# Performance work log

Measured on AMD Instinct MI355X. Metric: run time of the kernel, lower is better.

The kernel has to match this reference:

```python
import jax, jax.numpy as jnp
import numpy as np

B, T, N, H = 1024, 256, 32, 64  # batch, SEQ_LEN, N_SERIES, RNN_HID_SIZE
EPS = 1e-05


def setup_inputs() -> dict:
    key = jax.random.key(0)
    ks = jax.random.split(key, 24)
    s_h = 1.0 / np.sqrt(H)
    s_n = 1.0 / np.sqrt(N)
    u = lambda k, shape, s: jax.random.uniform(k, shape, jnp.float32, -s, s)
    inp = {
        'values': jax.random.normal(ks[0], (B, T, N), jnp.float32),
        'masks': (jax.random.uniform(ks[1], (B, T, N)) < 0.8).astype(jnp.float32),
        'deltas': jax.random.uniform(ks[2], (B, T, N), jnp.float32) * 5.0,
        'evals': jax.random.normal(ks[3], (B, T, N), jnp.float32),
        'eval_masks': (jax.random.uniform(ks[4], (B, T, N)) < 0.1).astype(jnp.float32),
        'labels': (jax.random.uniform(ks[5], (B, 1)) < 0.5).astype(jnp.float32),
        'is_train': jnp.ones((B, 1), jnp.float32),
        # TemporalDecay h: Linear(N->H)
        'td_h_W': u(ks[6], (H, N), s_h), 'td_h_b': u(ks[7], (H,), s_h),
        # TemporalDecay x: diag Linear(N->N)
        'td_x_W': u(ks[8], (N, N), s_n), 'td_x_b': u(ks[9], (N,), s_n),
        # hist_reg: Linear(H->N)
        'hist_W': u(ks[10], (N, H), s_n), 'hist_b': u(ks[11], (N,), s_n),
        # feat_reg: masked Linear(N->N), mask = 1 - I
        'feat_W': u(ks[12], (N, N), s_n), 'feat_b': u(ks[13], (N,), s_n),
        # weight_combine: Linear(2N->N)
        'wc_W': u(ks[14], (N, 2 * N), s_n), 'wc_b': u(ks[15], (N,), s_n),
        # LSTMCell(2N -> H)
        'W_ih': u(ks[16], (4 * H, 2 * N), s_h), 'W_hh': u(ks[17], (4 * H, H), s_h),
        'b_ih': u(ks[18], (4 * H,), s_h), 'b_hh': u(ks[19], (4 * H,), s_h),
        # out: Linear(H->1)
        'out_W': u(ks[20], (1, H), s_h), 'out_b': u(ks[21], (1,), s_h),
    }
    return inp


def _rits_forward(values, masks, deltas, labels, is_train,
                  td_h_W, td_h_b, td_x_W, td_x_b, hist_W, hist_b,
                  feat_W, feat_b, wc_W, wc_b, W_ih, W_hh, b_ih, b_hh,
                  out_W, out_b):
    # time-major for scan: [T, B, N]
    vals_t = jnp.swapaxes(values, 0, 1)
    masks_t = jnp.swapaxes(masks, 0, 1)
    delts_t = jnp.swapaxes(deltas, 0, 1)

    feat_mask = 1.0 - jnp.eye(N, dtype=values.dtype)
    td_x_diag = jnp.diagonal(td_x_W)                  # W * eye(N) linear == elementwise diag

    def step(carry, xmd):
        h, c, x_loss = carry
        x, m, d = xmd
        gamma_h = jnp.exp(-jax.nn.relu(d @ td_h_W.T + td_h_b))   # [B,H]
        gamma_x = jnp.exp(-jax.nn.relu(d * td_x_diag + td_x_b))  # [B,N]
        h = h * gamma_h
        x_h = h @ hist_W.T + hist_b
        msum = jnp.sum(m) + EPS
        x_loss = x_loss + jnp.sum(jnp.abs(x - x_h) * m) / msum
        x_c = m * x + (1.0 - m) * x_h
        z_h = x_c @ (feat_W * feat_mask).T + feat_b
        x_loss = x_loss + jnp.sum(jnp.abs(x - z_h) * m) / msum
        alpha = jnp.concatenate([gamma_x, m], axis=1) @ wc_W.T + wc_b
        c_h = alpha * z_h + (1.0 - alpha) * x_h
        x_loss = x_loss + jnp.sum(jnp.abs(x - c_h) * m) / msum
        c_c = m * x + (1.0 - m) * c_h
        inputs = jnp.concatenate([c_c, m], axis=1)  # [B, 2N]
        gates = inputs @ W_ih.T + b_ih + h @ W_hh.T + b_hh
        i, f, g, o = jnp.split(gates, 4, axis=1)
        c = jax.nn.sigmoid(f) * c + jax.nn.sigmoid(i) * jnp.tanh(g)
        h = jax.nn.sigmoid(o) * jnp.tanh(c)
        return (h, c, x_loss), c_c

    h0 = jnp.zeros((values.shape[0], H), values.dtype)
    c0 = jnp.zeros((values.shape[0], H), values.dtype)
    (h, c, x_loss), imps = jax.lax.scan(step, (h0, c0, jnp.float32(0.0)),
                                        (vals_t, masks_t, delts_t))
    imputations = jnp.swapaxes(imps, 0, 1)  # [B, T, N]

    y_h = h @ out_W.T + out_b  # logits [B,1]
    # binary_cross_entropy_with_logits, reduce=False
    max_val = jnp.maximum(-y_h, 0.0)
    bce = y_h - y_h * labels + max_val + jnp.log(jnp.exp(-max_val) + jnp.exp(-y_h - max_val))
    y_loss = jnp.sum(bce * is_train) / (jnp.sum(is_train) + EPS)
    loss = x_loss / T + y_loss * 0.1
    predictions = jax.nn.sigmoid(y_h)
    return loss, predictions, imputations


def reference(values, masks, deltas, evals, eval_masks, labels, is_train,
              td_h_W, td_h_b, td_x_W, td_x_b, hist_W, hist_b, feat_W, feat_b,
              wc_W, wc_b, W_ih, W_hh, b_ih, b_hh, out_W, out_b):
    loss, predictions, imputations = _rits_forward(
        values, masks, deltas, labels, is_train,
        td_h_W, td_h_b, td_x_W, td_x_b, hist_W, hist_b,
        feat_W, feat_b, wc_W, wc_b, W_ih, W_hh, b_ih, b_hh, out_W, out_b)
    return loss, predictions, imputations
```

## Files before the change

### kernel.cpp

```cpp
#include <hip/hip_runtime.h>

#define EPSF 1e-5f

typedef _Float16 h2f  __attribute__((ext_vector_type(2)));
typedef _Float16 h8   __attribute__((ext_vector_type(8)));
typedef float    f32x4 __attribute__((ext_vector_type(4)));

#if defined(__has_builtin)
#if __has_builtin(__builtin_amdgcn_fdot2)
#define HAVE_FDOT2 1
#endif
#endif

__device__ __forceinline__ float fsig(float x){ return 1.0f/(1.0f+__expf(-x)); }
__device__ __forceinline__ float ftanh(float x){
  float e = __expf(2.f*x);
  float r = (e-1.f)/(e+1.f);
  return (x > 15.f) ? 1.f : ((x < -15.f) ? -1.f : r);
}
__device__ __forceinline__ int pkf(float lo, float hi){
  return __builtin_bit_cast(int, __builtin_amdgcn_cvt_pkrtz(lo, hi));
}
__device__ __forceinline__ int4 mk4(const float* p){
  return make_int4(pkf(p[0],p[1]),pkf(p[2],p[3]),pkf(p[4],p[5]),pkf(p[6],p[7]));
}
__device__ __forceinline__ float dot2(int w, int x, float acc){
#ifdef HAVE_FDOT2
  return __builtin_amdgcn_fdot2(__builtin_bit_cast(h2f, w),
                                __builtin_bit_cast(h2f, x), acc, false);
#else
  h2f a = __builtin_bit_cast(h2f, w), b = __builtin_bit_cast(h2f, x);
  return acc + (float)a[0]*(float)b[0] + (float)a[1]*(float)b[1];
#endif
}
__device__ __forceinline__ int rl_i(int v, int l){ return __builtin_amdgcn_readlane(v, l); }
__device__ __forceinline__ float rl_f(float v, int l){
  return __int_as_float(__builtin_amdgcn_readlane(__float_as_int(v), l));
}
#define BAR() do{ asm volatile("s_waitcnt lgkmcnt(0)" ::: "memory"); __builtin_amdgcn_s_barrier(); }while(0)

__global__ void msum_kernel(const float* __restrict__ masks, float* __restrict__ msum){
  const int t   = blockIdx.x;
  const int tid = threadIdx.x;
  const int b0  = tid >> 3;
  const int n4  = (tid & 7) << 2;
  float s = 0.f;
  #pragma unroll 4
  for (int i = 0; i < 32; ++i) {
    const int b = b0 + (i << 5);
    const float4 v = *reinterpret_cast<const float4*>(masks + ((size_t)b*256 + t)*32 + n4);
    s += v.x + v.y + v.z + v.w;
  }
  __shared__ float red[256];
  red[tid] = s; __syncthreads();
  for (int off = 128; off > 0; off >>= 1) {
    if (tid < off) red[tid] += red[tid + off];
    __syncthreads();
  }
  if (tid == 0) msum[t] = red[0] + EPSF;
}

__global__ __launch_bounds__(512)
__attribute__((amdgpu_waves_per_eu(2, 2)))
void rits_kernel(
  const float* __restrict__ values, const float* __restrict__ masks,
  const float* __restrict__ deltas, const float* __restrict__ labels,
  const float* __restrict__ is_train,
  const float* __restrict__ td_h_W, const float* __restrict__ td_h_b,
  const float* __restrict__ td_x_W, const float* __restrict__ td_x_b,
  const float* __restrict__ hist_W, const float* __restrict__ hist_b,
  const float* __restrict__ feat_W, const float* __restrict__ feat_b,
  const float* __restrict__ wc_W,  const float* __restrict__ wc_b,
  const float* __restrict__ W_ih,  const float* __restrict__ W_hh,
  const float* __restrict__ b_ih,  const float* __restrict__ b_hh,
  const float* __restrict__ out_W, const float* __restrict__ out_b,
  const float* __restrict__ msum,
  float* __restrict__ xl_acc, float* __restrict__ bce_acc,
  float* __restrict__ predictions, float* __restrict__ imps)
{
  __shared__ __align__(16) int  inp_s[4][84];
  __shared__ float gp[4][256];
  __shared__ float msum_l[256];

  const int tid = threadIdx.x;
  const int b   = blockIdx.x;
  const int wv  = tid >> 6;
  const int ln  = tid & 63;
  const bool chain = (wv < 4);
  const int me  = wv & 3;
  const int b2  = (b << 2) | me;

  if (tid < 256) msum_l[tid] = 1.0f / msum[tid];

  int4 Wb[2][4];
  const int kg = ln >> 4;
  #pragma unroll
  for (int nt = 0; nt < 2; ++nt){
    const int col = (wv << 5) + (nt << 4) + (ln & 15);
    #pragma unroll
    for (int ks = 0; ks < 4; ++ks){
      const int k0 = (ks << 5) + (kg << 3);
      const float* src = (k0 < 64) ? (W_ih + (size_t)col*64 + k0)
                                   : (W_hh + (size_t)col*64 + (k0 - 64));
      Wb[nt][ks] = make_int4(pkf(src[0],src[1]), pkf(src[2],src[3]),
                             pkf(src[4],src[5]), pkf(src[6],src[7]));
    }
  }
  const int col0 = (wv << 5) + (ln & 15);
  const float bs0 = b_ih[col0]      + b_hh[col0];
  const float bs1 = b_ih[col0 + 16] + b_hh[col0 + 16];

  int4  fB[4];
  int4  fC[8];
  int4  fDa[8];
  float wz[32];
  float thb_r=0.f, tdxd_r=0.f, tdxb_r=0.f, histb_r=0.f, featb_r=0.f, wcb_r=0.f;
  float xv=0.f, mv=0.f, dv=0.f;
  if (chain){
    const int nr = ln & 31;
    #pragma unroll
    for (int g = 0; g < 4; ++g) fB[g] = mk4(td_h_W + ln*32 + 8*g);
    #pragma unroll
    for (int g = 0; g < 8; ++g) fC[g] = mk4(hist_W + nr*64 + 8*g);
    #pragma unroll
    for (int g = 0; g < 8; ++g) fDa[g] = mk4(wc_W + nr*64 + 8*g);
    #pragma unroll
    for (int k = 0; k < 32; ++k) wz[k] = (k==nr) ? 0.f : feat_W[nr*32 + k];
    thb_r = td_h_b[ln];
    if (ln < 32){
      tdxd_r  = td_x_W[ln*33];
      tdxb_r  = td_x_b[ln];
      histb_r = hist_b[ln];
      featb_r = feat_b[ln];
      wcb_r   = wc_b[ln];
      const size_t base = (size_t)b2*8192 + ln;
      xv = values[base]; mv = masks[base]; dv = deltas[base];
    }
  }
  float h_reg = 0.f, c_reg = 0.f, loss_acc = 0.f;

  __syncthreads();

  for (int t = 0; t < 256; ++t){
    if (chain){
      const float x_cur = xv, m_cur = mv, d_cur = dv;
      float gx_r = 0.f;
      if (ln < 32){
        gx_r = __expf(-fmaxf(fmaf(d_cur, tdxd_r, tdxb_r), 0.f));
        if (t < 255){
          const size_t base = (size_t)b2*8192 + (size_t)(t+1)*32 + ln;
          xv = values[base]; mv = masks[base]; dv = deltas[base];
        }
      }
      const int i0 = (2*ln) & 63, i1 = (2*ln+1) & 63;
      const int dw = pkf(__shfl(d_cur, i0), __shfl(d_cur, i1));
      const int j0 = (2*ln-32) & 63, j1 = (2*ln-31) & 63;
      const float ga  = __shfl(gx_r,  i0), gb  = __shfl(gx_r,  i1);
      const float ma_ = __shfl(m_cur, j0), mb_ = __shfl(m_cur, j1);
      const int aw = (ln < 16) ? pkf(ga, gb) : pkf(ma_, mb_);

      {
        float a0 = thb_r, a1 = 0.f;
        #pragma unroll
        for (int g4 = 0; g4 < 4; ++g4){
          const int4 w = fB[g4];
          a0 = dot2(w.x, rl_i(dw, 4*g4+0), a0);
          a1 = dot2(w.y, rl_i(dw, 4*g4+1), a1);
          a0 = dot2(w.z, rl_i(dw, 4*g4+2), a0);
          a1 = dot2(w.w, rl_i(dw, 4*g4+3), a1);
        }
        h_reg *= __expf(-fmaxf(a0+a1, 0.f));
      }
      const int hw = pkf(__shfl(h_reg, i0), __shfl(h_reg, i1));
      float xh_v = 0.f, x_c_v = 0.f;
      if (ln < 32){
        float a0 = histb_r, a1 = 0.f, a2 = 0.f, a3 = 0.f;
        #pragma unroll
        for (int g4 = 0; g4 < 8; ++g4){
          const int4 w = fC[g4];
          a0 = dot2(w.x, rl_i(hw, 4*g4+0), a0);
          a1 = dot2(w.y, rl_i(hw, 4*g4+1), a1);
          a2 = dot2(w.z, rl_i(hw, 4*g4+2), a2);
          a3 = dot2(w.w, rl_i(hw, 4*g4+3), a3);
        }
        xh_v  = (a0+a1)+(a2+a3);
        x_c_v = m_cur*x_cur + (1.f-m_cur)*xh_v;
      }
      float ccv = 0.f;
      if (ln < 32){
        float z0 = featb_r, z1 = 0.f, z2 = 0.f, z3 = 0.f;
        #pragma unroll
        for (int k = 0; k < 32; k += 4){
          z0 = fmaf(rl_f(x_c_v, k+0), wz[k+0], z0);
          z1 = fmaf(rl_f(x_c_v, k+1), wz[k+1], z1);
          z2 = fmaf(rl_f(x_c_v, k+2), wz[k+2], z2);
          z3 = fmaf(rl_f(x_c_v, k+3), wz[k+3], z3);
        }
        const float z = (z0+z1)+(z2+z3);
        float a0 = wcb_r, a1 = 0.f, a2 = 0.f, a3 = 0.f;
        #pragma unroll
        for (int g4 = 0; g4 < 8; ++g4){
          const int4 w = fDa[g4];
          a0 = dot2(w.x, rl_i(aw, 4*g4+0), a0);
          a1 = dot2(w.y, rl_i(aw, 4*g4+1), a1);
          a2 = dot2(w.z, rl_i(aw, 4*g4+2), a2);
          a3 = dot2(w.w, rl_i(aw, 4*g4+3), a3);
        }
        const float al = (a0+a1)+(a2+a3);
        const float ch = al*z + (1.f-al)*xh_v;
        loss_acc += (fabsf(x_cur-xh_v)+fabsf(x_cur-z)+fabsf(x_cur-ch))*m_cur*msum_l[t];
        ccv = m_cur*x_cur + (1.f-m_cur)*ch;
        imps[(size_t)b2*8192 + (size_t)t*32 + ln] = ccv;
      }
      const int ccw = pkf(__shfl(ccv, i0), __shfl(ccv, i1));
      inp_s[me][ln] = (ln < 16) ? ccw : (ln < 32 ? aw : hw);
    }

    BAR();

    {
      const int arow = ln & 15;
      int4 A[4];
      if (arow < 4){
        #pragma unroll
        for (int ks = 0; ks < 4; ++ks)
          A[ks] = *reinterpret_cast<const int4*>(&inp_s[arow][(ks << 4) + (kg << 2)]);
      } else {
        #pragma unroll
        for (int ks = 0; ks < 4; ++ks) A[ks] = make_int4(0,0,0,0);
      }
      f32x4 acc0 = {bs0, bs0, bs0, bs0};
      f32x4 acc1 = {bs1, bs1, bs1, bs1};
      #pragma unroll
      for (int ks = 0; ks < 4; ++ks){
        acc0 = __builtin_amdgcn_mfma_f32_16x16x32_f16(
                 __builtin_bit_cast(h8, A[ks]), __builtin_bit_cast(h8, Wb[0][ks]), acc0, 0,0,0);
        acc1 = __builtin_amdgcn_mfma_f32_16x16x32_f16(
                 __builtin_bit_cast(h8, A[ks]), __builtin_bit_cast(h8, Wb[1][ks]), acc1, 0,0,0);
      }
      if (kg == 0){
        #pragma unroll
        for (int e = 0; e < 4; ++e){
          gp[e][col0]      = acc0[e];
          gp[e][col0 + 16] = acc1[e];
        }
      }
    }

    BAR();

    if (chain){
      const float ig = gp[me][ln];
      const float fg = gp[me][64+ln];
      const float gg = gp[me][128+ln];
      const float og = gp[me][192+ln];
      c_reg = fsig(fg)*c_reg + fsig(ig)*ftanh(gg);
      h_reg = fsig(og)*ftanh(c_reg);
    }
  }

  if (chain){
    float l = loss_acc;
    l += __shfl_xor(l,16); l += __shfl_xor(l,8);
    l += __shfl_xor(l,4);  l += __shfl_xor(l,2); l += __shfl_xor(l,1);
    if (ln == 0) atomicAdd(xl_acc, l);

    float p = h_reg * out_W[ln];
    p += __shfl_xor(p,32); p += __shfl_xor(p,16); p += __shfl_xor(p,8);
    p += __shfl_xor(p,4);  p += __shfl_xor(p,2);  p += __shfl_xor(p,1);
    if (ln == 0){
      const float y = p + out_b[0];
      predictions[b2] = fsig(y);
      const float lab = labels[b2];
      const float it  = is_train[b2];
      const float mx  = fmaxf(-y, 0.f);
      const float bce = y - y*lab + mx + __logf(__expf(-mx) + __expf(-y - mx));
      atomicAdd(bce_acc, bce * it);
    }
  }
}

__global__ void final_kernel(const float* __restrict__ is_train,
                             const float* __restrict__ ws,
                             float* __restrict__ out){
  const int tid = threadIdx.x;
  __shared__ float red[256];
  red[tid] = is_train[tid] + is_train[tid+256] + is_train[tid+512] + is_train[tid+768];
  __syncthreads();
  for (int off = 128; off > 0; off >>= 1){
    if (tid < off) red[tid] += red[tid + off];
    __syncthreads();
  }
  if (tid == 0){
    const float yl = ws[1] / (red[0] + EPSF);
    out[0] = ws[0] / 256.0f + 0.1f * yl;
  }
}

extern "C" void kernel_launch(void* const* d_in, const int* in_sizes, int n_in,
                              void* d_out, int out_size, void* d_ws, size_t ws_size,
                              hipStream_t stream){
  const float* values   = (const float*)d_in[0];
  const float* masks    = (const float*)d_in[1];
  const float* deltas   = (const float*)d_in[2];
  const float* labels   = (const float*)d_in[5];
  const float* is_train = (const float*)d_in[6];
  const float* td_h_W   = (const float*)d_in[7];
  const float* td_h_b   = (const float*)d_in[8];
  const float* td_x_W   = (const float*)d_in[9];
  const float* td_x_b   = (const float*)d_in[10];
  const float* hist_W   = (const float*)d_in[11];
  const float* hist_b   = (const float*)d_in[12];
  const float* feat_W   = (const float*)d_in[13];
  const float* feat_b   = (const float*)d_in[14];
  const float* wc_W     = (const float*)d_in[15];
  const float* wc_b     = (const float*)d_in[16];
  const float* W_ih     = (const float*)d_in[17];
  const float* W_hh     = (const float*)d_in[18];
  const float* b_ih     = (const float*)d_in[19];
  const float* b_hh     = (const float*)d_in[20];
  const float* out_W    = (const float*)d_in[21];
  const float* out_b    = (const float*)d_in[22];

  float* out = (float*)d_out;
  float* ws  = (float*)d_ws;

  hipMemsetAsync(ws, 0, 2*sizeof(float), stream);
  msum_kernel<<<256, 256, 0, stream>>>(masks, ws + 2);
  rits_kernel<<<256, 512, 0, stream>>>(values, masks, deltas, labels, is_train,
      td_h_W, td_h_b, td_x_W, td_x_b, hist_W, hist_b, feat_W, feat_b,
      wc_W, wc_b, W_ih, W_hh, b_ih, b_hh, out_W, out_b,
      ws + 2, ws + 0, ws + 1, out + 1, out + 1 + 1024);
  final_kernel<<<1, 256, 0, stream>>>(is_train, ws, out);
}
```

Measured before the change: 449.7 us.

## Offload temporal-decay hidden projection to idle waves via MFMA one step ahead

The td_h decay matmul (delta to H) moves off the serial chain waves. The non-chain waves (wv>=4) compute it with one MFMA per step for the next timestep, using packed deltas staged in shared memory. Chain waves now read the precomputed pre-activation from shared memory instead of doing 16 dot2+readlane ops on the critical path. This costs extra shared-memory traffic and an MFMA on the helper waves between the two barriers.

Measured after the change: 441.7 us. Within noise of the previous version (-1.8%).

```diff
diff --git a/kernel.cpp b/kernel.cpp
--- a/kernel.cpp
+++ b/kernel.cpp
@@ -37,6 +37,8 @@
 __device__ __forceinline__ float rl_f(float v, int l){
   return __int_as_float(__builtin_amdgcn_readlane(__float_as_int(v), l));
 }
+#define MFMA(A,B,C) __builtin_amdgcn_mfma_f32_16x16x32_f16( \
+    __builtin_bit_cast(h8,(A)), __builtin_bit_cast(h8,(B)), (C), 0,0,0)
 #define BAR() do{ asm volatile("s_waitcnt lgkmcnt(0)" ::: "memory"); __builtin_amdgcn_s_barrier(); }while(0)
 
 __global__ void msum_kernel(const float* __restrict__ masks, float* __restrict__ msum){
@@ -79,6 +81,8 @@
   float* __restrict__ predictions, float* __restrict__ imps)
 {
   __shared__ __align__(16) int  inp_s[4][84];
+  __shared__ __align__(16) int  dw_s[4][20];
+  __shared__ float sB[4][64];
   __shared__ float gp[4][256];
   __shared__ float msum_l[256];
 
@@ -89,11 +93,12 @@
   const bool chain = (wv < 4);
   const int me  = wv & 3;
   const int b2  = (b << 2) | me;
+  const int kg  = ln >> 4;
+  const int arow = ln & 15;
 
   if (tid < 256) msum_l[tid] = 1.0f / msum[tid];
 
   int4 Wb[2][4];
-  const int kg = ln >> 4;
   #pragma unroll
   for (int nt = 0; nt < 2; ++nt){
     const int col = (wv << 5) + (nt << 4) + (ln & 15);
@@ -110,23 +115,27 @@
   const float bs0 = b_ih[col0]      + b_hh[col0];
   const float bs1 = b_ih[col0 + 16] + b_hh[col0 + 16];
 
-  int4  fB[4];
+  int4 fGh = make_int4(0,0,0,0);
+  float ghb = 0.f; int colj = 0;
+  if (wv >= 4){
+    colj = ((wv - 4) << 4) | (ln & 15);
+    fGh  = mk4(td_h_W + colj*32 + kg*8);
+    ghb  = td_h_b[colj];
+  }
+
   int4  fC[8];
   int4  fDa[8];
   float wz[32];
-  float thb_r=0.f, tdxd_r=0.f, tdxb_r=0.f, histb_r=0.f, featb_r=0.f, wcb_r=0.f;
+  float tdxd_r=0.f, tdxb_r=0.f, histb_r=0.f, featb_r=0.f, wcb_r=0.f;
   float xv=0.f, mv=0.f, dv=0.f;
   if (chain){
     const int nr = ln & 31;
-    #pragma unroll
-    for (int g = 0; g < 4; ++g) fB[g] = mk4(td_h_W + ln*32 + 8*g);
     #pragma unroll
     for (int g = 0; g < 8; ++g) fC[g] = mk4(hist_W + nr*64 + 8*g);
     #pragma unroll
     for (int g = 0; g < 8; ++g) fDa[g] = mk4(wc_W + nr*64 + 8*g);
     #pragma unroll
     for (int k = 0; k < 32; ++k) wz[k] = (k==nr) ? 0.f : feat_W[nr*32 + k];
-    thb_r = td_h_b[ln];
     if (ln < 32){
       tdxd_r  = td_x_W[ln*33];
       tdxb_r  = td_x_b[ln];
@@ -138,12 +147,32 @@
     }
   }
   float h_reg = 0.f, c_reg = 0.f, loss_acc = 0.f;
-
+  const int i0 = (2*ln) & 63, i1 = (2*ln+1) & 63;
+  const int j0 = (2*ln-32) & 63, j1 = (2*ln-31) & 63;
+
+  __syncthreads();
+
+  if (chain){
+    const int dwn = pkf(__shfl(dv, i0), __shfl(dv, i1));
+    if (ln < 16) dw_s[me][ln] = dwn;
+  }
+  __syncthreads();
+  if (wv >= 4){
+    int4 A = make_int4(0,0,0,0);
+    if (arow < 4) A = *reinterpret_cast<const int4*>(&dw_s[arow][kg << 2]);
+    f32x4 acc = {ghb, ghb, ghb, ghb};
+    acc = MFMA(A, fGh, acc);
+    if (kg == 0){
+      #pragma unroll
+      for (int e = 0; e < 4; ++e) sB[e][colj] = acc[e];
+    }
+  }
   __syncthreads();
 
   for (int t = 0; t < 256; ++t){
     if (chain){
       const float x_cur = xv, m_cur = mv, d_cur = dv;
+      const float sb = sB[me][ln];
       float gx_r = 0.f;
       if (ln < 32){
         gx_r = __expf(-fmaxf(fmaf(d_cur, tdxd_r, tdxb_r), 0.f));
@@ -152,25 +181,11 @@
           xv = values[base]; mv = masks[base]; dv = deltas[base];
         }
       }
-      const int i0 = (2*ln) & 63, i1 = (2*ln+1) & 63;
-      const int dw = pkf(__shfl(d_cur, i0), __shfl(d_cur, i1));
-      const int j0 = (2*ln-32) & 63, j1 = (2*ln-31) & 63;
-      const float ga  = __shfl(gx_r,  i0), gb  = __shfl(gx_r,  i1);
+      const float ga  = __shfl(gx_r,  i0), gb_ = __shfl(gx_r,  i1);
       const float ma_ = __shfl(m_cur, j0), mb_ = __shfl(m_cur, j1);
-      const int aw = (ln < 16) ? pkf(ga, gb) : pkf(ma_, mb_);
-
-      {
-        float a0 = thb_r, a1 = 0.f;
-        #pragma unroll
-        for (int g4 = 0; g4 < 4; ++g4){
-          const int4 w = fB[g4];
-          a0 = dot2(w.x, rl_i(dw, 4*g4+0), a0);
-          a1 = dot2(w.y, rl_i(dw, 4*g4+1), a1);
-          a0 = dot2(w.z, rl_i(dw, 4*g4+2), a0);
-          a1 = dot2(w.w, rl_i(dw, 4*g4+3), a1);
-        }
-        h_reg *= __expf(-fmaxf(a0+a1, 0.f));
-      }
+      const int aw = (ln < 16) ? pkf(ga, gb_) : pkf(ma_, mb_);
+
+      h_reg *= __expf(-fmaxf(sb, 0.f));
       const int hw = pkf(__shfl(h_reg, i0), __shfl(h_reg, i1));
       float xh_v = 0.f, x_c_v = 0.f;
       if (ln < 32){
@@ -214,12 +229,15 @@
       }
       const int ccw = pkf(__shfl(ccv, i0), __shfl(ccv, i1));
       inp_s[me][ln] = (ln < 16) ? ccw : (ln < 32 ? aw : hw);
+      if (t < 255){
+        const int dwn = pkf(__shfl(dv, i0), __shfl(dv, i1));
+        if (ln < 16) dw_s[me][ln] = dwn;
+      }
     }
 
     BAR();
 
     {
-      const int arow = ln & 15;
       int4 A[4];
       if (arow < 4){
         #pragma unroll
@@ -244,6 +262,16 @@
           gp[e][col0]      = acc0[e];
           gp[e][col0 + 16] = acc1[e];
         }
+      }
+    }
+    if (wv >= 4){
+      int4 Agh = make_int4(0,0,0,0);
+      if (arow < 4) Agh = *reinterpret_cast<const int4*>(&dw_s[arow][kg << 2]);
+      f32x4 accg = {ghb, ghb, ghb, ghb};
+      accg = MFMA(Agh, fGh, accg);
+      if (kg == 0){
+        #pragma unroll
+        for (int e = 0; e < 4; ++e) sB[e][colj] = accg[e];
       }
     }
 
```
